# Kernel tuning notes

Measured on AMD Instinct MI355X. Metric: run time of the kernel, lower is better.

Reference implementation:

```python
import jax, jax.numpy as jnp
import numpy as np

B, S, DM, H, DF = 2, 2048, 1024, 16, 4096
HD = DM // H
EPS = 1e-6
NEG = -1e9


def setup_inputs() -> dict:
    key = jax.random.key(0)
    ks = jax.random.split(key, 16)
    sc = 1.0 / np.sqrt(DM)
    scf = 1.0 / np.sqrt(DF)
    return {
        "x": jax.random.normal(ks[0], (B, S, DM), jnp.float32),
        "src_mask": jax.random.randint(ks[1], (B, 1, 1, S), 0, 2, jnp.int32),
        "Wq": jax.random.normal(ks[2], (DM, DM), jnp.float32) * sc,
        "bq": jnp.zeros((DM,), jnp.float32),
        "Wk": jax.random.normal(ks[3], (DM, DM), jnp.float32) * sc,
        "bk": jnp.zeros((DM,), jnp.float32),
        "Wv": jax.random.normal(ks[4], (DM, DM), jnp.float32) * sc,
        "bv": jnp.zeros((DM,), jnp.float32),
        "Wo": jax.random.normal(ks[5], (DM, DM), jnp.float32) * sc,
        "bo": jnp.zeros((DM,), jnp.float32),
        "W1": jax.random.normal(ks[6], (DM, DF), jnp.float32) * sc,
        "b1": jnp.zeros((DF,), jnp.float32),
        "W2": jax.random.normal(ks[7], (DF, DM), jnp.float32) * scf,
        "b2": jnp.zeros((DM,), jnp.float32),
        "alpha1": jnp.ones((1,), jnp.float32),
        "beta1": jnp.ones((1,), jnp.float32),
        "alpha2": jnp.ones((1,), jnp.float32),
        "beta2": jnp.ones((1,), jnp.float32),
    }


def layer_norm(x, alpha, beta):
    # torch: mean + unbiased std (ddof=1), scalar alpha/beta, eps added to std
    mean = jnp.mean(x, axis=-1, keepdims=True)
    std = jnp.std(x, axis=-1, keepdims=True, ddof=1)
    return alpha * (x - mean) / (std + EPS) + beta


def mha(x, mask, Wq, bq, Wk, bk, Wv, bv, Wo, bo):
    def split(t):  # [B,S,DM] -> [B,H,S,HD]
        return t.reshape(B, S, H, HD).transpose(0, 2, 1, 3)
    q = split(x @ Wq + bq)
    k = split(x @ Wk + bk)
    v = split(x @ Wv + bv)
    scores = jnp.einsum("bhqd,bhkd->bhqk", q, k) / np.sqrt(HD)
    scores = jnp.where(mask == 0, NEG, scores)
    probs = jax.nn.softmax(scores, axis=-1)  # dropout in eval mode = identity
    out = jnp.einsum("bhqk,bhkd->bhqd", probs, v)
    out = out.transpose(0, 2, 1, 3).reshape(B, S, DM)
    return out @ Wo + bo


def reference(x, src_mask, Wq, bq, Wk, bk, Wv, bv, Wo, bo, W1, b1, W2, b2,
              alpha1, beta1, alpha2, beta2):
    # pre-norm residual: x + attn(norm(x)); dropout disabled (eval)
    n1 = layer_norm(x, alpha1, beta1)
    h = x + mha(n1, src_mask, Wq, bq, Wk, bk, Wv, bv, Wo, bo)
    n2 = layer_norm(h, alpha2, beta2)
    ff = jax.nn.relu(n2 @ W1 + b1) @ W2 + b2
    return h + ff
```

## Files before the change

### kernel.cpp

```cpp
#include <hip/hip_runtime.h>
#include <hip/hip_bf16.h>

#define SEQ   2048
#define BATCH 2
#define DMODEL 1024
#define DFF   4096
#define NHEAD 16
#define HDIM  64
#define NTOK  (BATCH*SEQ)

typedef short s8v __attribute__((ext_vector_type(8)));
typedef float f4v __attribute__((ext_vector_type(4)));

__device__ __forceinline__ float b2f(unsigned short u) {
    union { unsigned int i; float f; } v; v.i = ((unsigned int)u) << 16; return v.f;
}
__device__ __forceinline__ unsigned short f2b(float f) {
    union { unsigned int i; float f; } v; v.f = f;
    unsigned int r = v.i + 0x7FFFu + ((v.i >> 16) & 1u);
    return (unsigned short)(r >> 16);
}
__device__ __forceinline__ ushort2 cvt_pk(float a, float b) {
    __hip_bfloat162 h = __float22bfloat162_rn(float2{ a, b });
    return *(ushort2*)&h;
}

__device__ __forceinline__ f4v mfma_bf16(s8v a, s8v b, f4v c) {
    return __builtin_amdgcn_mfma_f32_16x16x32_bf16(a, b, c, 0, 0, 0);
}

__device__ __forceinline__ void gload_lds16(const void* g, void* l) {
    __builtin_amdgcn_global_load_lds(
        (const __attribute__((address_space(1))) unsigned int*)g,
        (__attribute__((address_space(3))) unsigned int*)l, 16, 0, 0);
}

template<int N> __device__ __forceinline__ void wait_vmcnt() {
    if constexpr (N == 8)      asm volatile("s_waitcnt vmcnt(8)" ::: "memory");
    else if constexpr (N == 6) asm volatile("s_waitcnt vmcnt(6)" ::: "memory");
    else if constexpr (N == 2) asm volatile("s_waitcnt vmcnt(2)" ::: "memory");
    else                       asm volatile("s_waitcnt vmcnt(0)" ::: "memory");
}

__device__ __forceinline__ void tp_tile(const float* __restrict__ src,
                                        unsigned short* __restrict__ dst,
                                        int R, int C, int br, int bc, int t,
                                        unsigned short* tl) {
    for (int i = 0; i < 16; i++) {
        int idx = t + 256 * i;
        int r = idx >> 6, c = idx & 63;
        tl[r * 65 + c] = f2b(src[(size_t)(br * 64 + r) * C + bc * 64 + c]);
    }
    __syncthreads();
    for (int i = 0; i < 16; i++) {
        int idx = t + 256 * i;
        int r2 = idx >> 6, c2 = idx & 63;
        dst[(size_t)(bc * 64 + r2) * R + br * 64 + c2] = tl[c2 * 65 + r2];
    }
}

__global__ __launch_bounds__(256) void prep_weights(const float* __restrict__ Wq,
                                                    const float* __restrict__ Wk,
                                                    const float* __restrict__ Wv,
                                                    const float* __restrict__ Wo,
                                                    const float* __restrict__ W1,
                                                    const float* __restrict__ W2,
                                                    const float* __restrict__ bq,
                                                    const float* __restrict__ bk,
                                                    const float* __restrict__ bv,
                                                    const int* __restrict__ msk,
                                                    const float* __restrict__ x,
                                                    const float* __restrict__ a1,
                                                    const float* __restrict__ be1,
                                                    unsigned short* __restrict__ Wqkv_t,
                                                    unsigned short* __restrict__ Wo_t,
                                                    unsigned short* __restrict__ W1_t,
                                                    unsigned short* __restrict__ W2_t,
                                                    float* __restrict__ bqkv,
                                                    float* __restrict__ maskf,
                                                    unsigned short* __restrict__ n1) {
    __shared__ unsigned short tl[64 * 65];
    __shared__ float red[8];
    const int t = threadIdx.x;
    const int bx = blockIdx.x, by = blockIdx.y, z = blockIdx.z;
    if (z < 4) {
        const float* src = (z == 0) ? Wq : (z == 1) ? Wk : (z == 2) ? Wv : Wo;
        unsigned short* dst = (z == 3) ? Wo_t : Wqkv_t + (size_t)z * 1024 * 1024;
        tp_tile(src, dst, 1024, 1024, bx, by, t, tl);
    } else if (z == 4) {
        for (int i = 0; i < 4; i++) {
            tp_tile(W1, W1_t, 1024, 4096, bx, by + 16 * i, t, tl);
            __syncthreads();
        }
    } else if (z == 5) {
        if (bx == 0 && by == 0) {
            for (int i = 0; i < 12; i++) {
                int idx = t + 256 * i;
                if (idx < 1024) bqkv[idx] = bq[idx];
                else if (idx < 2048) bqkv[idx] = bk[idx - 1024];
                else if (idx < 3072) bqkv[idx] = bv[idx - 2048];
            }
        }
        if (bx == 1 && by == 0) {
            for (int i = 0; i < 16; i++) {
                int idx = t + 256 * i;
                maskf[idx] = (msk[idx] == 0) ? -1e9f : 0.f;
            }
        }
        for (int i = 0; i < 4; i++) {
            tp_tile(W2, W2_t, 4096, 1024, bx + 16 * i, by, t, tl);
            __syncthreads();
        }
    } else {
        const int row = (z - 6) * 256 + by * 16 + bx;
        const float* xr = x + (size_t)row * DMODEL;
        float4 u = ((const float4*)xr)[t];
        float v[4] = { u.x, u.y, u.z, u.w };
        float s = v[0] + v[1] + v[2] + v[3];
        float sq = v[0]*v[0] + v[1]*v[1] + v[2]*v[2] + v[3]*v[3];
        for (int off = 32; off; off >>= 1) { s += __shfl_xor(s, off); sq += __shfl_xor(sq, off); }
        int wave = t >> 6, lane = t & 63;
        if (!lane) { red[wave] = s; red[4 + wave] = sq; }
        __syncthreads();
        s = red[0] + red[1] + red[2] + red[3];
        sq = red[4] + red[5] + red[6] + red[7];
        float mean = s * (1.f / DMODEL);
        float var = (sq - (float)DMODEL * mean * mean) * (1.f / (DMODEL - 1));
        var = var < 0.f ? 0.f : var;
        float inv = a1[0] / (sqrtf(var) + 1e-6f);
        float bt = be1[0];
        uint2 ou;
        unsigned short r0 = f2b((v[0] - mean) * inv + bt);
        unsigned short r1 = f2b((v[1] - mean) * inv + bt);
        unsigned short r2 = f2b((v[2] - mean) * inv + bt);
        unsigned short r3 = f2b((v[3] - mean) * inv + bt);
        ou.x = (unsigned int)r0 | ((unsigned int)r1 << 16);
        ou.y = (unsigned int)r2 | ((unsigned int)r3 << 16);
        ((uint2*)(n1 + (size_t)row * DMODEL))[t] = ou;
    }
}

__global__ __launch_bounds__(256) void pack_kv(const unsigned short* __restrict__ Kb,
                                               const unsigned short* __restrict__ Vb,
                                               unsigned short* __restrict__ Kc,
                                               unsigned short* __restrict__ Vc) {
    __shared__ unsigned short tl[64 * 65];
    const int t = threadIdx.x;
    const int kt = blockIdx.x, h = blockIdx.y, b = blockIdx.z;
    const unsigned short* srcK = Kb + (size_t)b * SEQ * 1024 + h * HDIM;
    unsigned short* dstK = Kc + ((size_t)((b * NHEAD + h) * 32 + kt)) * 4096;
    for (int i = 0; i < 2; i++) {
        int ci = t + 256 * i;
        int r = ci >> 3, cp = ci & 7;
        int cl = cp ^ (r & 7);
        *(uint4*)&dstK[ci * 8] = *(const uint4*)&srcK[(size_t)(kt * 64 + r) * 1024 + cl * 8];
    }
    const unsigned short* srcV = Vb + (size_t)b * SEQ * 1024 + h * HDIM;
    for (int i = 0; i < 16; i++) {
        int idx = t + 256 * i;
        int r = idx >> 6, c = idx & 63;
        tl[r * 65 + c] = srcV[(size_t)(kt * 64 + r) * 1024 + c];
    }
    __syncthreads();
    unsigned short* dstV = Vc + ((size_t)((b * NHEAD + h) * 32 + kt)) * 4096;
    for (int i = 0; i < 2; i++) {
        int ci = t + 256 * i;
        int r = ci >> 3, cp = ci & 7;
        int cl = cp ^ (r & 7);
        ushort4 e0, e1;
        e0.x = tl[(cl * 8 + 0) * 65 + r]; e0.y = tl[(cl * 8 + 1) * 65 + r];
        e0.z = tl[(cl * 8 + 2) * 65 + r]; e0.w = tl[(cl * 8 + 3) * 65 + r];
        e1.x = tl[(cl * 8 + 4) * 65 + r]; e1.y = tl[(cl * 8 + 5) * 65 + r];
        e1.z = tl[(cl * 8 + 6) * 65 + r]; e1.w = tl[(cl * 8 + 7) * 65 + r];
        *(ushort4*)&dstV[ci * 8]     = e0;
        *(ushort4*)&dstV[ci * 8 + 4] = e1;
    }
}

__global__ __launch_bounds__(256) void ln_kernel(const float* __restrict__ x,
                                                 const float* __restrict__ al,
                                                 const float* __restrict__ be,
                                                 unsigned short* __restrict__ o) {
    const int row = blockIdx.x;
    const float* xr = x + (size_t)row * DMODEL;
    float4 u = ((const float4*)xr)[threadIdx.x];
    float v[4] = { u.x, u.y, u.z, u.w };
    float s = v[0] + v[1] + v[2] + v[3];
    float sq = v[0]*v[0] + v[1]*v[1] + v[2]*v[2] + v[3]*v[3];
    for (int off = 32; off; off >>= 1) { s += __shfl_xor(s, off); sq += __shfl_xor(sq, off); }
    __shared__ float red[8];
    int wave = threadIdx.x >> 6, lane = threadIdx.x & 63;
    if (!lane) { red[wave] = s; red[4 + wave] = sq; }
    __syncthreads();
    s = red[0] + red[1] + red[2] + red[3];
    sq = red[4] + red[5] + red[6] + red[7];
    float mean = s * (1.f / DMODEL);
    float var = (sq - (float)DMODEL * mean * mean) * (1.f / (DMODEL - 1));
    var = var < 0.f ? 0.f : var;
    float inv = al[0] / (sqrtf(var) + 1e-6f);
    float bt = be[0];
    uint2 ou;
    unsigned short r0 = f2b((v[0] - mean) * inv + bt);
    unsigned short r1 = f2b((v[1] - mean) * inv + bt);
    unsigned short r2 = f2b((v[2] - mean) * inv + bt);
    unsigned short r3 = f2b((v[3] - mean) * inv + bt);
    ou.x = (unsigned int)r0 | ((unsigned int)r1 << 16);
    ou.y = (unsigned int)r2 | ((unsigned int)r3 << 16);
    ((uint2*)(o + (size_t)row * DMODEL))[threadIdx.x] = ou;
}

template<int BROWS>
__device__ __forceinline__ void stage256(const unsigned short* __restrict__ A,
                                         const unsigned short* __restrict__ Bt,
                                         int m0, int n0, int K, int k0,
                                         unsigned short* sA, unsigned short* sB, int t) {
#pragma unroll
    for (int i = 0; i < 4; i++) {
        int ci = i * 512 + t;
        int r = ci >> 3, c = (ci & 7) ^ (r & 7);
        gload_lds16(A + (size_t)(m0 + r) * K + k0 + c * 8, sA + (size_t)ci * 8);
    }
#pragma unroll
    for (int i = 0; i < BROWS / 64; i++) {
        int ci = i * 512 + t;
        int r = ci >> 3, c = (ci & 7) ^ (r & 7);
        gload_lds16(Bt + (size_t)(n0 + r) * K + k0 + c * 8, sB + (size_t)ci * 8);
    }
}

template<int NFC>
__device__ __forceinline__ void comp256(const unsigned short* sA, const unsigned short* sB,
                                        int wm, int wn, int l16, int quad,
                                        f4v acc[8][NFC]) {
#pragma unroll
    for (int s = 0; s < 2; s++) {
        s8v b[NFC];
#pragma unroll
        for (int ni = 0; ni < NFC; ni++) {
            int r = wn * (NFC * 16) + ni * 16 + l16;
            int p = (s * 4 + quad) ^ (r & 7);
            b[ni] = *(const s8v*)&sB[r * 64 + p * 8];
        }
#pragma unroll
        for (int mi = 0; mi < 8; mi++) {
            int r = wm * 128 + mi * 16 + l16;
            int p = (s * 4 + quad) ^ (r & 7);
            s8v a = *(const s8v*)&sA[r * 64 + p * 8];
#pragma unroll
            for (int ni = 0; ni < NFC; ni++)
                acc[mi][ni] = mfma_bf16(a, b[ni], acc[mi][ni]);
        }
    }
}

template<bool RELU, bool RES, typename CT, bool SPLIT3, int BN>
__global__ __launch_bounds__(512, 2) void gemm256(const unsigned short* __restrict__ A,
                                                  const unsigned short* __restrict__ Bt,
                                                  const float* __restrict__ bias,
                                                  const float* __restrict__ res,
                                                  CT* __restrict__ C,
                                                  float* __restrict__ pbuf,
                                                  int M, int N, int K, int KS) {
    constexpr int NFC = BN / 64;
    constexpr int LPT = 4 + BN / 64;
    __shared__ __align__(16) unsigned short smA[2][256 * 64];
    __shared__ __align__(16) unsigned short smB[2][BN * 64];
    const int t = threadIdx.x;
    const int wave = t >> 6, lane = t & 63;
    const int quad = lane >> 4, l16 = lane & 15;
    const int wm = wave >> 2, wn = wave & 3;
    const int m0 = blockIdx.x * 256, n0 = blockIdx.y * BN;
    const int z = blockIdx.z;
    const int kbeg = z * KS;
    const int nt = KS >> 6;

    f4v acc[8][NFC] = {};

    stage256<BN>(A, Bt, m0, n0, K, kbeg,      smA[0], smB[0], t);
    stage256<BN>(A, Bt, m0, n0, K, kbeg + 64, smA[1], smB[1], t);
    wait_vmcnt<LPT>();
    __builtin_amdgcn_s_barrier();

    for (int it = 0; it < nt - 2; ++it) {
        const int cb = it & 1;
        __builtin_amdgcn_s_setprio(1);
        comp256<NFC>(smA[cb], smB[cb], wm, wn, l16, quad, acc);
        __builtin_amdgcn_s_setprio(0);
        asm volatile("s_waitcnt lgkmcnt(0)" ::: "memory");
        __builtin_amdgcn_s_barrier();
        stage256<BN>(A, Bt, m0, n0, K, kbeg + (it + 2) * 64, smA[cb], smB[cb], t);
        wait_vmcnt<LPT>();
        __builtin_amdgcn_s_barrier();
    }
    {
        const int cb = (nt - 2) & 1;
        __builtin_amdgcn_s_setprio(1);
        comp256<NFC>(smA[cb], smB[cb], wm, wn, l16, quad, acc);
        __builtin_amdgcn_s_setprio(0);
        asm volatile("s_waitcnt vmcnt(0)" ::: "memory");
        __builtin_amdgcn_s_barrier();
    }
    {
        const int cb = (nt - 1) & 1;
        __builtin_amdgcn_s_setprio(1);
        comp256<NFC>(smA[cb], smB[cb], wm, wn, l16, quad, acc);
        __builtin_amdgcn_s_setprio(0);
    }

#pragma unroll
    for (int mi = 0; mi < 8; mi++) {
#pragma unroll
        for (int ni = 0; ni < NFC; ni++) {
            const int col = n0 + wn * (NFC * 16) + ni * 16 + l16;
            const int row0 = m0 + wm * 128 + mi * 16 + quad * 4;
            if (z == 0) {
                const float bv = bias[col];
#pragma unroll
                for (int r = 0; r < 4; r++) {
                    float v = acc[mi][ni][r] + bv;
                    if (RELU) v = v > 0.f ? v : 0.f;
                    if (RES) v += res[(size_t)(row0 + r) * N + col];
                    size_t cidx;
                    if constexpr (SPLIT3)
                        cidx = (size_t)(col >> 10) * ((size_t)NTOK * 1024)
                             + (size_t)(row0 + r) * 1024 + (col & 1023);
                    else
                        cidx = (size_t)(row0 + r) * N + col;
                    if constexpr (sizeof(CT) == 2)
                        C[cidx] = f2b(v);
                    else
                        C[cidx] = v;
                }
            } else {
#pragma unroll
                for (int r = 0; r < 4; r++)
                    pbuf[(size_t)(z - 1) * M * N + (size_t)(row0 + r) * N + col]
                        = acc[mi][ni][r];
            }
        }
    }
}

__global__ __launch_bounds__(256) void add_pbuf(float* __restrict__ out,
                                                const float* __restrict__ pbuf) {
    const int i0 = (blockIdx.x * 256 + threadIdx.x) * 8;
    float4 a0 = *(const float4*)&out[i0];
    float4 a1 = *(const float4*)&out[i0 + 4];
    float4 p0 = *(const float4*)&pbuf[i0];
    float4 p1 = *(const float4*)&pbuf[i0 + 4];
    a0.x += p0.x; a0.y += p0.y; a0.z += p0.z; a0.w += p0.w;
    a1.x += p1.x; a1.y += p1.y; a1.z += p1.z; a1.w += p1.w;
    *(float4*)&out[i0]     = a0;
    *(float4*)&out[i0 + 4] = a1;
}

__device__ __forceinline__ void attn_tile(const unsigned short* __restrict__ smKb,
                                          const unsigned short* __restrict__ smVb,
                                          const float* __restrict__ smM, int k0,
                                          unsigned short* __restrict__ smPw,
                                          s8v qf0, s8v qf1, int quad, int l16,
                                          float& l_s, f4v* oacc) {
    const int l7 = l16 & 7;
    f4v s[4];
#pragma unroll
    for (int kt4 = 0; kt4 < 4; kt4++) {
        int r = kt4 * 16 + l16;
        s8v kf0 = *(const s8v*)&smKb[r * 64 + ((quad ^ l7) * 8)];
        s8v kf1 = *(const s8v*)&smKb[r * 64 + (((quad + 4) ^ l7) * 8)];
        f4v z = {};
        z = mfma_bf16(kf0, qf0, z);
        z = mfma_bf16(kf1, qf1, z);
        s[kt4] = z;
    }
#pragma unroll
    for (int kt4 = 0; kt4 < 4; kt4++) {
        float4 mf = *(const float4*)&smM[k0 + kt4 * 16 + quad * 4];
        s[kt4][0] = s[kt4][0] * 0.125f + mf.x;
        s[kt4][1] = s[kt4][1] * 0.125f + mf.y;
        s[kt4][2] = s[kt4][2] * 0.125f + mf.z;
        s[kt4][3] = s[kt4][3] * 0.125f + mf.w;
    }
#pragma unroll
    for (int kt4 = 0; kt4 < 4; kt4++)
#pragma unroll
        for (int r = 0; r < 4; r++) {
            float p = __expf(s[kt4][r]);
            s[kt4][r] = p;
            l_s += p;
        }
#pragma unroll
    for (int kt4 = 0; kt4 < 4; kt4++) {
        ushort2 p01 = cvt_pk(s[kt4][0], s[kt4][1]);
        ushort2 p23 = cvt_pk(s[kt4][2], s[kt4][3]);
        ushort4 pk;
        pk.x = p01.x; pk.y = p01.y; pk.z = p23.x; pk.w = p23.y;
        int c = kt4 * 2 + (quad >> 1);
        *(ushort4*)&smPw[l16 * 64 + ((c ^ l7) * 8 + (quad & 1) * 4)] = pk;
    }
    s8v pf0 = *(const s8v*)&smPw[l16 * 64 + ((quad ^ l7) * 8)];
    s8v pf1 = *(const s8v*)&smPw[l16 * 64 + (((quad + 4) ^ l7) * 8)];
#pragma unroll
    for (int nt = 0; nt < 4; nt++) {
        int r = nt * 16 + l16;
        s8v v0 = *(const s8v*)&smVb[r * 64 + ((quad ^ l7) * 8)];
        s8v v1 = *(const s8v*)&smVb[r * 64 + (((quad + 4) ^ l7) * 8)];
        oacc[nt] = mfma_bf16(pf0, v0, oacc[nt]);
        oacc[nt] = mfma_bf16(pf1, v1, oacc[nt]);
    }
}

__global__ __launch_bounds__(512) void attn_kernel(const unsigned short* __restrict__ Qb,
                                                   const unsigned short* __restrict__ Kc,
                                                   const unsigned short* __restrict__ Vc,
                                                   const float* __restrict__ maskf,
                                                   unsigned short* __restrict__ out) {
    __shared__ __align__(16) unsigned short smK[2][4096];
    __shared__ __align__(16) unsigned short smV[2][4096];
    __shared__ __align__(16) unsigned short smP[8][1024];
    __shared__ __align__(16) float smM[SEQ];

    const int t = threadIdx.x;
    const int wave = t >> 6, lane = t & 63;
    const int quad = lane >> 4, l16 = lane & 15;
    const int qt = blockIdx.x, h = blockIdx.y, b = blockIdx.z;
    const int q0 = qt * 128 + wave * 16;
    const unsigned short* Kbh = Kc + ((size_t)(b * NHEAD + h)) * 32 * 4096;
    const unsigned short* Vbh = Vc + ((size_t)(b * NHEAD + h)) * 32 * 4096;
    unsigned short* smPw = &smP[wave][0];

    const unsigned short* Qp = Qb + ((size_t)b * SEQ + q0 + l16) * 1024 + h * HDIM + quad * 8;
    s8v qf0 = *(const s8v*)(Qp);
    s8v qf1 = *(const s8v*)(Qp + 32);

    gload_lds16(maskf + (size_t)b * SEQ + t * 4, (float*)smM + t * 4);
    gload_lds16(Kbh + t * 8,        smK[0] + t * 8);
    gload_lds16(Vbh + t * 8,        smV[0] + t * 8);
    gload_lds16(Kbh + 4096 + t * 8, smK[1] + t * 8);
    gload_lds16(Vbh + 4096 + t * 8, smV[1] + t * 8);
    wait_vmcnt<2>();
    __builtin_amdgcn_s_barrier();

    float l_s = 0.f;
    f4v oacc[4] = {};

    for (int it = 0; it < 30; ++it) {
        const int cb = it & 1;
        __builtin_amdgcn_s_setprio(1);
        attn_tile(smK[cb], smV[cb], smM, it * 64, smPw, qf0, qf1, quad, l16, l_s, oacc);
        __builtin_amdgcn_s_setprio(0);
        asm volatile("s_waitcnt lgkmcnt(0)" ::: "memory");
        __builtin_amdgcn_s_barrier();
        gload_lds16(Kbh + (size_t)(it + 2) * 4096 + t * 8, smK[cb] + t * 8);
        gload_lds16(Vbh + (size_t)(it + 2) * 4096 + t * 8, smV[cb] + t * 8);
        wait_vmcnt<2>();
        __builtin_amdgcn_s_barrier();
    }
    {
        __builtin_amdgcn_s_setprio(1);
        attn_tile(smK[0], smV[0], smM, 30 * 64, smPw, qf0, qf1, quad, l16, l_s, oacc);
        __builtin_amdgcn_s_setprio(0);
        wait_vmcnt<0>();
        __builtin_amdgcn_s_barrier();
    }
    {
        __builtin_amdgcn_s_setprio(1);
        attn_tile(smK[1], smV[1], smM, 31 * 64, smPw, qf0, qf1, quad, l16, l_s, oacc);
        __builtin_amdgcn_s_setprio(0);
    }

    l_s += __shfl_xor(l_s, 16);
    l_s += __shfl_xor(l_s, 32);
    float lrr[4];
    for (int r = 0; r < 4; r++) lrr[r] = __shfl(l_s, quad * 4 + r);
    for (int nt = 0; nt < 4; nt++)
        for (int r = 0; r < 4; r++) {
            int row = q0 + quad * 4 + r;
            int col = h * HDIM + nt * 16 + l16;
            out[((size_t)b * SEQ + row) * DMODEL + col] = f2b(oacc[nt][r] / lrr[r]);
        }
}

extern "C" void kernel_launch(void* const* d_in, const int* in_sizes, int n_in,
                              void* d_out, int out_size, void* d_ws, size_t ws_size,
                              hipStream_t stream) {
    const float* x   = (const float*)d_in[0];
    const int*   msk = (const int*)d_in[1];
    const float* Wq  = (const float*)d_in[2];
    const float* bq  = (const float*)d_in[3];
    const float* Wk  = (const float*)d_in[4];
    const float* bk  = (const float*)d_in[5];
    const float* Wv  = (const float*)d_in[6];
    const float* bv  = (const float*)d_in[7];
    const float* Wo  = (const float*)d_in[8];
    const float* bo  = (const float*)d_in[9];
    const float* W1  = (const float*)d_in[10];
    const float* b1  = (const float*)d_in[11];
    const float* W2  = (const float*)d_in[12];
    const float* b2  = (const float*)d_in[13];
    const float* a1  = (const float*)d_in[14];
    const float* be1 = (const float*)d_in[15];
    const float* a2  = (const float*)d_in[16];
    const float* be2 = (const float*)d_in[17];
    float* outf = (float*)d_out;

    char* ws = (char*)d_ws;
    const size_t MB = 1024 * 1024;
    unsigned short* W2_t   = (unsigned short*)(ws);
    unsigned short* W1_t   = (unsigned short*)(ws + 8 * MB);
    float*          Pbuf   = (float*)(ws + 8 * MB);
    unsigned short* Wqkv_t = (unsigned short*)(ws + 16 * MB);
    float*          bqkv   = (float*)(ws + 22 * MB);
    unsigned short* Kc     = (unsigned short*)(ws + 16 * MB);
    unsigned short* n2     = (unsigned short*)(ws + 16 * MB);
    unsigned short* Wo_t   = (unsigned short*)(ws + 24 * MB);
    unsigned short* Qb     = (unsigned short*)(ws + 26 * MB);
    unsigned short* Kb     = (unsigned short*)(ws + 34 * MB);
    unsigned short* Vb     = (unsigned short*)(ws + 42 * MB);
    float*          Pbuf2  = (float*)(ws + 34 * MB);
    unsigned short* ff1    = (unsigned short*)(ws + 26 * MB);
    unsigned short* attnO  = (unsigned short*)(ws + 50 * MB);
    unsigned short* n1     = (unsigned short*)d_out;
    float*          maskf  = (float*)((char*)d_out + 8 * MB);
    unsigned short* Vc     = (unsigned short*)d_out;
    float*          hbuf   = (float*)d_out;

    prep_weights<<<dim3(16, 16, 22), 256, 0, stream>>>(
        Wq, Wk, Wv, Wo, W1, W2, bq, bk, bv, msk, x, a1, be1,
        Wqkv_t, Wo_t, W1_t, W2_t, bqkv, maskf, n1);

    gemm256<false, false, unsigned short, true, 256><<<dim3(16, 12, 1), 512, 0, stream>>>(
        n1, Wqkv_t, bqkv, nullptr, Qb, nullptr, NTOK, 3072, 1024, 1024);
    pack_kv<<<dim3(32, 16, 2), 256, 0, stream>>>(Kb, Vb, Kc, Vc);
    attn_kernel<<<dim3(16, 16, 2), 512, 0, stream>>>(Qb, Kc, Vc, maskf, attnO);
    gemm256<false, true, float, false, 128><<<dim3(16, 8, 2), 512, 0, stream>>>(
        attnO, Wo_t, bo, x, hbuf, Pbuf2, NTOK, 1024, 1024, 512);
    add_pbuf<<<dim3(2048), 256, 0, stream>>>(hbuf, Pbuf2);
    ln_kernel<<<NTOK, 256, 0, stream>>>(hbuf, a2, be2, n2);
    gemm256<true, false, unsigned short, false, 256><<<dim3(16, 16, 1), 512, 0, stream>>>(
        n2, W1_t, b1, nullptr, ff1, nullptr, NTOK, DFF, 1024, 1024);
    gemm256<false, true, float, false, 128><<<dim3(16, 8, 2), 512, 0, stream>>>(
        ff1, W2_t, b2, hbuf, outf, Pbuf, NTOK, 1024, 4096, 2048);
    add_pbuf<<<dim3(2048), 256, 0, stream>>>(outf, Pbuf);
}
```

Before: 372.4 us.

## Compact unmasked keys and skip fully masked key tiles in attention

Adds a per-batch prefix-scan kernel that builds a compacted index list of unmasked key positions and a tile count. pack_kv now gathers only those K/V rows, and the attention loop runs only over the compacted tiles, so masked keys that contribute exactly zero probability are never processed. The softmax exponent also switches to exp2 with the log2(e) factor folded into the scale constant. This adds a small scan kernel and gather loads, and a fully masked batch (zero tiles) would divide by zero instead of matching the reference's uniform distribution.

```diff
diff --git a/kernel.cpp b/kernel.cpp
--- a/kernel.cpp
+++ b/kernel.cpp
@@ -68,7 +68,6 @@
                                                     const float* __restrict__ bq,
                                                     const float* __restrict__ bk,
                                                     const float* __restrict__ bv,
-                                                    const int* __restrict__ msk,
                                                     const float* __restrict__ x,
                                                     const float* __restrict__ a1,
                                                     const float* __restrict__ be1,
@@ -77,7 +76,6 @@
                                                     unsigned short* __restrict__ W1_t,
                                                     unsigned short* __restrict__ W2_t,
                                                     float* __restrict__ bqkv,
-                                                    float* __restrict__ maskf,
                                                     unsigned short* __restrict__ n1) {
     __shared__ unsigned short tl[64 * 65];
     __shared__ float red[8];
@@ -99,12 +97,6 @@
                 if (idx < 1024) bqkv[idx] = bq[idx];
                 else if (idx < 2048) bqkv[idx] = bk[idx - 1024];
                 else if (idx < 3072) bqkv[idx] = bv[idx - 2048];
-            }
-        }
-        if (bx == 1 && by == 0) {
-            for (int i = 0; i < 16; i++) {
-                int idx = t + 256 * i;
-                maskf[idx] = (msk[idx] == 0) ? -1e9f : 0.f;
             }
         }
         for (int i = 0; i < 4; i++) {
@@ -140,26 +132,69 @@
     }
 }
 
+__global__ __launch_bounds__(256) void mask_scan(const int* __restrict__ msk,
+                                                 int* __restrict__ idx,
+                                                 float* __restrict__ maskc2,
+                                                 int* __restrict__ ntiles) {
+    const int b = blockIdx.x, t = threadIdx.x;
+    const int base = b * SEQ;
+    __shared__ int wsum[4];
+    int k[8]; int cnt = 0;
+    for (int j = 0; j < 8; j++) {
+        k[j] = (msk[base + t * 8 + j] != 0) ? 1 : 0;
+        cnt += k[j];
+    }
+    const int lane = t & 63, wv = t >> 6;
+    int pre = cnt;
+    for (int off = 1; off < 64; off <<= 1) {
+        int n = __shfl_up(pre, off);
+        if (lane >= off) pre += n;
+    }
+    if (lane == 63) wsum[wv] = pre;
+    __syncthreads();
+    const int Nb = wsum[0] + wsum[1] + wsum[2] + wsum[3];
+    int woff = 0;
+    for (int w = 0; w < wv; w++) woff += wsum[w];
+    const int excl = woff + pre - cnt;
+    for (int j = 0; j < 8; j++) {
+        int g = t * 8 + j;
+        idx[base + g] = 0;
+        maskc2[base + g] = (g < Nb) ? 0.f : -1e9f;
+    }
+    __syncthreads();
+    int pos = excl;
+    for (int j = 0; j < 8; j++) {
+        if (k[j]) { idx[base + pos] = t * 8 + j; pos++; }
+    }
+    if (t == 0) ntiles[b] = (Nb + 63) >> 6;
+}
+
 __global__ __launch_bounds__(256) void pack_kv(const unsigned short* __restrict__ Kb,
                                                const unsigned short* __restrict__ Vb,
+                                               const int* __restrict__ idx,
+                                               const int* __restrict__ ntiles,
                                                unsigned short* __restrict__ Kc,
                                                unsigned short* __restrict__ Vc) {
     __shared__ unsigned short tl[64 * 65];
     const int t = threadIdx.x;
     const int kt = blockIdx.x, h = blockIdx.y, b = blockIdx.z;
+    if (kt >= ntiles[b]) return;
+    const int* idxb = idx + b * SEQ + kt * 64;
     const unsigned short* srcK = Kb + (size_t)b * SEQ * 1024 + h * HDIM;
     unsigned short* dstK = Kc + ((size_t)((b * NHEAD + h) * 32 + kt)) * 4096;
     for (int i = 0; i < 2; i++) {
         int ci = t + 256 * i;
         int r = ci >> 3, cp = ci & 7;
         int cl = cp ^ (r & 7);
-        *(uint4*)&dstK[ci * 8] = *(const uint4*)&srcK[(size_t)(kt * 64 + r) * 1024 + cl * 8];
+        int row = idxb[r];
+        *(uint4*)&dstK[ci * 8] = *(const uint4*)&srcK[(size_t)row * 1024 + cl * 8];
     }
     const unsigned short* srcV = Vb + (size_t)b * SEQ * 1024 + h * HDIM;
     for (int i = 0; i < 16; i++) {
-        int idx = t + 256 * i;
-        int r = idx >> 6, c = idx & 63;
-        tl[r * 65 + c] = srcV[(size_t)(kt * 64 + r) * 1024 + c];
+        int idx2 = t + 256 * i;
+        int r = idx2 >> 6, c = idx2 & 63;
+        int row = idxb[r];
+        tl[r * 65 + c] = srcV[(size_t)row * 1024 + c];
     }
     __syncthreads();
     unsigned short* dstV = Vc + ((size_t)((b * NHEAD + h) * 32 + kt)) * 4096;
@@ -354,6 +389,7 @@
     *(float4*)&out[i0 + 4] = a1;
 }
 
+#define EXPC 0.18033688f
 __device__ __forceinline__ void attn_tile(const unsigned short* __restrict__ smKb,
                                           const unsigned short* __restrict__ smVb,
                                           const float* __restrict__ smM, int k0,
@@ -375,16 +411,16 @@
 #pragma unroll
     for (int kt4 = 0; kt4 < 4; kt4++) {
         float4 mf = *(const float4*)&smM[k0 + kt4 * 16 + quad * 4];
-        s[kt4][0] = s[kt4][0] * 0.125f + mf.x;
-        s[kt4][1] = s[kt4][1] * 0.125f + mf.y;
-        s[kt4][2] = s[kt4][2] * 0.125f + mf.z;
-        s[kt4][3] = s[kt4][3] * 0.125f + mf.w;
+        s[kt4][0] = s[kt4][0] * EXPC + mf.x;
+        s[kt4][1] = s[kt4][1] * EXPC + mf.y;
+        s[kt4][2] = s[kt4][2] * EXPC + mf.z;
+        s[kt4][3] = s[kt4][3] * EXPC + mf.w;
     }
 #pragma unroll
     for (int kt4 = 0; kt4 < 4; kt4++)
 #pragma unroll
         for (int r = 0; r < 4; r++) {
-            float p = __expf(s[kt4][r]);
+            float p = __builtin_amdgcn_exp2f(s[kt4][r]);
             s[kt4][r] = p;
             l_s += p;
         }
@@ -412,7 +448,8 @@
 __global__ __launch_bounds__(512) void attn_kernel(const unsigned short* __restrict__ Qb,
                                                    const unsigned short* __restrict__ Kc,
                                                    const unsigned short* __restrict__ Vc,
-                                                   const float* __restrict__ maskf,
+                                                   const float* __restrict__ maskc2,
+                                                   const int* __restrict__ ntiles,
                                                    unsigned short* __restrict__ out) {
     __shared__ __align__(16) unsigned short smK[2][4096];
     __shared__ __align__(16) unsigned short smV[2][4096];
@@ -424,6 +461,7 @@
     const int quad = lane >> 4, l16 = lane & 15;
     const int qt = blockIdx.x, h = blockIdx.y, b = blockIdx.z;
     const int q0 = qt * 128 + wave * 16;
+    const int nt = ntiles[b];
     const unsigned short* Kbh = Kc + ((size_t)(b * NHEAD + h)) * 32 * 4096;
     const unsigned short* Vbh = Vc + ((size_t)(b * NHEAD + h)) * 32 * 4096;
     unsigned short* smPw = &smP[wave][0];
@@ -432,7 +470,7 @@
     s8v qf0 = *(const s8v*)(Qp);
     s8v qf1 = *(const s8v*)(Qp + 32);
 
-    gload_lds16(maskf + (size_t)b * SEQ + t * 4, (float*)smM + t * 4);
+    gload_lds16(maskc2 + (size_t)b * SEQ + t * 4, (float*)smM + t * 4);
     gload_lds16(Kbh + t * 8,        smK[0] + t * 8);
     gload_lds16(Vbh + t * 8,        smV[0] + t * 8);
     gload_lds16(Kbh + 4096 + t * 8, smK[1] + t * 8);
@@ -443,40 +481,35 @@
     float l_s = 0.f;
     f4v oacc[4] = {};
 
-    for (int it = 0; it < 30; ++it) {
+    for (int it = 0; it < nt; ++it) {
         const int cb = it & 1;
         __builtin_amdgcn_s_setprio(1);
         attn_tile(smK[cb], smV[cb], smM, it * 64, smPw, qf0, qf1, quad, l16, l_s, oacc);
         __builtin_amdgcn_s_setprio(0);
-        asm volatile("s_waitcnt lgkmcnt(0)" ::: "memory");
-        __builtin_amdgcn_s_barrier();
-        gload_lds16(Kbh + (size_t)(it + 2) * 4096 + t * 8, smK[cb] + t * 8);
-        gload_lds16(Vbh + (size_t)(it + 2) * 4096 + t * 8, smV[cb] + t * 8);
-        wait_vmcnt<2>();
-        __builtin_amdgcn_s_barrier();
-    }
-    {
-        __builtin_amdgcn_s_setprio(1);
-        attn_tile(smK[0], smV[0], smM, 30 * 64, smPw, qf0, qf1, quad, l16, l_s, oacc);
-        __builtin_amdgcn_s_setprio(0);
-        wait_vmcnt<0>();
-        __builtin_amdgcn_s_barrier();
-    }
-    {
-        __builtin_amdgcn_s_setprio(1);
-        attn_tile(smK[1], smV[1], smM, 31 * 64, smPw, qf0, qf1, quad, l16, l_s, oacc);
-        __builtin_amdgcn_s_setprio(0);
+        if (it + 2 < nt) {
+            asm volatile("s_waitcnt lgkmcnt(0)" ::: "memory");
+            __builtin_amdgcn_s_barrier();
+            gload_lds16(Kbh + (size_t)(it + 2) * 4096 + t * 8, smK[cb] + t * 8);
+            gload_lds16(Vbh + (size_t)(it + 2) * 4096 + t * 8, smV[cb] + t * 8);
+            wait_vmcnt<2>();
+            __builtin_amdgcn_s_barrier();
+        } else if (it + 1 < nt) {
+            asm volatile("s_waitcnt lgkmcnt(0)" ::: "memory");
+            __builtin_amdgcn_s_barrier();
+            wait_vmcnt<0>();
+            __builtin_amdgcn_s_barrier();
+        }
     }
 
     l_s += __shfl_xor(l_s, 16);
     l_s += __shfl_xor(l_s, 32);
     float lrr[4];
     for (int r = 0; r < 4; r++) lrr[r] = __shfl(l_s, quad * 4 + r);
-    for (int nt = 0; nt < 4; nt++)
+    for (int nt2 = 0; nt2 < 4; nt2++)
         for (int r = 0; r < 4; r++) {
             int row = q0 + quad * 4 + r;
-            int col = h * HDIM + nt * 16 + l16;
-            out[((size_t)b * SEQ + row) * DMODEL + col] = f2b(oacc[nt][r] / lrr[r]);
+            int col = h * HDIM + nt2 * 16 + l16;
+            out[((size_t)b * SEQ + row) * DMODEL + col] = f2b(oacc[nt2][r] / lrr[r]);
         }
 }
 
@@ -520,18 +553,21 @@
     unsigned short* ff1    = (unsigned short*)(ws + 26 * MB);
     unsigned short* attnO  = (unsigned short*)(ws + 50 * MB);
     unsigned short* n1     = (unsigned short*)d_out;
-    float*          maskf  = (float*)((char*)d_out + 8 * MB);
     unsigned short* Vc     = (unsigned short*)d_out;
     float*          hbuf   = (float*)d_out;
-
+    float*          maskc2 = (float*)((char*)d_out + 8 * MB);
+    int*            idxc   = (int*)((char*)d_out + 8 * MB + 16 * 1024);
+    int*            ntl    = (int*)((char*)d_out + 8 * MB + 32 * 1024);
+
+    mask_scan<<<dim3(BATCH), 256, 0, stream>>>(msk, idxc, maskc2, ntl);
     prep_weights<<<dim3(16, 16, 22), 256, 0, stream>>>(
-        Wq, Wk, Wv, Wo, W1, W2, bq, bk, bv, msk, x, a1, be1,
-        Wqkv_t, Wo_t, W1_t, W2_t, bqkv, maskf, n1);
+        Wq, Wk, Wv, Wo, W1, W2, bq, bk, bv, x, a1, be1,
+        Wqkv_t, Wo_t, W1_t, W2_t, bqkv, n1);
 
     gemm256<false, false, unsigned short, true, 256><<<dim3(16, 12, 1), 512, 0, stream>>>(
         n1, Wqkv_t, bqkv, nullptr, Qb, nullptr, NTOK, 3072, 1024, 1024);
-    pack_kv<<<dim3(32, 16, 2), 256, 0, stream>>>(Kb, Vb, Kc, Vc);
-    attn_kernel<<<dim3(16, 16, 2), 512, 0, stream>>>(Qb, Kc, Vc, maskf, attnO);
+    pack_kv<<<dim3(32, 16, 2), 256, 0, stream>>>(Kb, Vb, idxc, ntl, Kc, Vc);
+    attn_kernel<<<dim3(16, 16, 2), 512, 0, stream>>>(Qb, Kc, Vc, maskc2, ntl, attnO);
     gemm256<false, true, float, false, 128><<<dim3(16, 8, 2), 512, 0, stream>>>(
         attnO, Wo_t, bo, x, hbuf, Pbuf2, NTOK, 1024, 1024, 512);
     add_pbuf<<<dim3(2048), 256, 0, stream>>>(hbuf, Pbuf2);
```

Result: faster. 353.1 us (-5.2%).
